# Optimization experiments

Measured on AMD Instinct MI355X. Metric: run time of the kernel, lower is better.

Reference implementation:

```python
import jax, jax.numpy as jnp
import numpy as np

B, T, IN_DIM, OUT_DIM, H = 2, 256, 512, 256, 8
TEMP = 1.0
BN_EPS = 1e-5


def _boundary_mask(bnd):
    # bnd: (B, T) float in {0,1}. Vectorized version of the nested-loop
    # construction: mask[j,k] = prod_{m=min(j,k)..max(j,k)} (1 - bnd[m]), diag=1.
    q = 1.0 - bnd  # (B, T)
    ar = jnp.arange(T)

    def per_batch(qb):
        def row(j):
            # cumprod of q starting at position j (entries before j treated as 1)
            return jnp.cumprod(jnp.where(ar >= j, qb, 1.0))
        M = jax.vmap(row)(ar)                 # (T, T); valid for k >= j
        upper = ar[None, :] >= ar[:, None]
        full = jnp.where(upper, M, M.T)       # symmetrize
        eye = ar[None, :] == ar[:, None]
        return jnp.where(eye, 1.0, full)      # diagonal forced to 1

    return jax.vmap(per_batch)(q)             # (B, T, T)


def setup_inputs() -> dict:
    key = jax.random.key(0)
    ks = jax.random.split(key, 8)
    s_in = 1.0 / np.sqrt(IN_DIM)
    s_hin = 1.0 / np.sqrt(H * IN_DIM)
    return {
        "x": jax.random.normal(ks[0], (B, T, IN_DIM), dtype=jnp.float32),
        "boundary": jax.random.randint(ks[1], (B, T), 0, 2, dtype=jnp.int32),
        "att_proj_w": jax.random.normal(ks[2], (OUT_DIM, IN_DIM), dtype=jnp.float32) * s_in,
        "att_proj_b": jnp.zeros((OUT_DIM,), dtype=jnp.float32),
        "att_weight": jax.random.normal(ks[3], (OUT_DIM, H), dtype=jnp.float32) * (1.0 / np.sqrt(OUT_DIM)),
        "proj_att_w": jax.random.normal(ks[4], (OUT_DIM, H * IN_DIM), dtype=jnp.float32) * s_hin,
        "proj_att_b": jnp.zeros((OUT_DIM,), dtype=jnp.float32),
        "proj_noatt_w": jax.random.normal(ks[5], (OUT_DIM, IN_DIM), dtype=jnp.float32) * s_in,
        "proj_noatt_b": jnp.zeros((OUT_DIM,), dtype=jnp.float32),
        "bn_gamma": jnp.ones((OUT_DIM,), dtype=jnp.float32),
        "bn_beta": jnp.zeros((OUT_DIM,), dtype=jnp.float32),
    }


def reference(x, boundary, att_proj_w, att_proj_b, att_weight,
              proj_att_w, proj_att_b, proj_noatt_w, proj_noatt_b,
              bn_gamma, bn_beta):
    bnd = boundary.astype(x.dtype)

    # pairwise node products: (B, T, T, IN_DIM)
    pm = x[:, :, None, :] * x[:, None, :, :]
    # attention logits: tanh(Linear) @ att_weight -> (B, T, T, H)
    a = jnp.tanh(jnp.einsum('bjkd,od->bjko', pm, att_proj_w) + att_proj_b)
    att = jnp.einsum('bjko,oh->bjkh', a, att_weight) / TEMP

    # boundary message-control mask, then softmax over the key-node axis (dim=-2)
    mask = _boundary_mask(bnd)                 # (B, T, T)
    att = att * mask[..., None]
    att = jax.nn.softmax(att, axis=-2)

    # aggregate per head; torch flattens (IN_DIM, H) -> IN_DIM*H with d-major order
    x1 = jnp.einsum('bjkh,bkd->bjdh', att, x).reshape(x.shape[0], x.shape[1], -1)
    x1 = x1 @ proj_att_w.T + proj_att_b
    x2 = x @ proj_noatt_w.T + proj_noatt_b
    y = x1 + x2                                # (B, T, OUT_DIM)

    # BatchNorm1d in training mode over flattened (B*T, OUT_DIM), biased variance
    flat = y.reshape(-1, y.shape[-1])
    mu = flat.mean(axis=0)
    var = flat.var(axis=0)
    yn = (flat - mu) * jax.lax.rsqrt(var + BN_EPS) * bn_gamma + bn_beta
    return jax.nn.selu(yn.reshape(y.shape))
```

## Files before the change

### kernel.cpp

```cpp
#include <hip/hip_runtime.h>
#include <hip/hip_bf16.h>

#define B_ 2
#define T_ 256
#define D_ 512
#define O_ 256
#define H_ 8

typedef __attribute__((ext_vector_type(4))) float f32x4;
typedef __attribute__((ext_vector_type(8))) short bf16x8;
typedef unsigned short u16;
typedef unsigned int u32;

__device__ __forceinline__ u16 f2b(float f) {
    u32 u = __builtin_bit_cast(u32, f);
    u32 r = (u + 0x7FFFu + ((u >> 16) & 1u)) >> 16;
    return (u16)r;
}
__device__ __forceinline__ u32 cvtpk(float lo, float hi) {
    u32 r;
    asm("v_cvt_pk_bf16_f32 %0, %1, %2" : "=v"(r) : "v"(lo), "v"(hi));
    return r;
}
__device__ __forceinline__ float fast_tanh(float x) {
    float ax = fabsf(x);
    float e = __expf(-2.f * ax);
    float r = (1.f - e) / (1.f + e);
    return x < 0.f ? -r : r;
}
__device__ __forceinline__ uint4 ld8f2b(const float* __restrict__ p) {
    f32x4 a = *reinterpret_cast<const f32x4*>(p);
    f32x4 b = *reinterpret_cast<const f32x4*>(p + 4);
    uint4 pk;
    pk.x = cvtpk(a[0], a[1]);
    pk.y = cvtpk(a[2], a[3]);
    pk.z = cvtpk(b[0], b[1]);
    pk.w = cvtpk(b[2], b[3]);
    return pk;
}
__device__ __forceinline__ void gload16(const void* g, void* l) {
    __builtin_amdgcn_global_load_lds(
        (const __attribute__((address_space(1))) unsigned int*)g,
        (__attribute__((address_space(3))) unsigned int*)l, 16, 0, 0);
}

__global__ void k0_prep(const float* __restrict__ x, const float* __restrict__ W2,
                        u16* __restrict__ Xbf, u16* __restrict__ W2t) {
    const int tid = threadIdx.x;
    if (blockIdx.x < 64) {
        int base = (blockIdx.x * 256 + tid) * 16;
        uint4 o0 = ld8f2b(x + base);
        uint4 o1 = ld8f2b(x + base + 8);
        *reinterpret_cast<uint4*>(Xbf + base) = o0;
        *reinterpret_cast<uint4*>(Xbf + base + 8) = o1;
        return;
    }
    const int bx2 = blockIdx.x - 64;
    const int o0 = (bx2 >> 3) * 16;
    const int dc = bx2 & 7;
    __shared__ u16 TL[8192];
    #pragma unroll
    for (int c = 0; c < 8; ++c) {
        int i = tid * 32 + c * 4;
        int r = i >> 9, rem = i & 511;
        f32x4 v = *reinterpret_cast<const f32x4*>(
            W2 + (size_t)(o0 + r) * 4096 + dc * 512 + rem);
        int dd = rem >> 3, h0 = rem & 7;
        TL[(h0 + 0) * 1024 + r * 64 + dd] = f2b(v[0]);
        TL[(h0 + 1) * 1024 + r * 64 + dd] = f2b(v[1]);
        TL[(h0 + 2) * 1024 + r * 64 + dd] = f2b(v[2]);
        TL[(h0 + 3) * 1024 + r * 64 + dd] = f2b(v[3]);
    }
    __syncthreads();
    #pragma unroll
    for (int c = 0; c < 4; ++c) {
        int jj = tid * 32 + c * 8;
        int h = jj >> 10, r = (jj >> 6) & 15, dd = jj & 63;
        *reinterpret_cast<uint4*>(W2t + (size_t)(h * 256 + o0 + r) * 512 + dc * 64 + dd) =
            *reinterpret_cast<const uint4*>(&TL[jj]);
    }
}

__launch_bounds__(256, 3)
__global__ void k1a_att(const u16* __restrict__ Xbf, const float* __restrict__ xf,
                        const float* __restrict__ Wap, const float* __restrict__ bap,
                        const float* __restrict__ aw, float* __restrict__ attpart)
{
    const int oc = blockIdx.x & 3;
    const int j = (blockIdx.x >> 2) & 255;
    const int b = blockIdx.x >> 10;
    const int jt = j >> 6;
    const int tid = threadIdx.x;
    const int w = tid >> 6;
    const int l = tid & 63;
    const int l15 = l & 15;
    const int lgp = l >> 4;
    const bool act = (w >= jt);

    __shared__ __align__(16) u16 XL[256 * 64];
    __shared__ __align__(16) u16 WL[64 * 72];
    __shared__ __align__(16) u16 awT[16 * 72];
    __shared__ float xj[512];

    const u16* xb = Xbf + b * (T_ * D_);
    const float* xjp = xf + (b * T_ + j) * D_;
    for (int i = tid; i < D_; i += 256) xj[i] = xjp[i];
    for (int i = tid; i < 16 * 72; i += 256) awT[i] = 0;
    __syncthreads();
    for (int i = tid; i < 64 * 8; i += 256) {
        int ol = i >> 3, h = i & 7;
        awT[h * 72 + ol] = f2b(aw[(oc * 64 + ol) * 8 + h]);
    }

    const int srow_off = (l >> 3);
    const int scol = ((l & 7) ^ ((l >> 3) & 7)) * 8;
    const int i0 = jt * 2;

    f32x4 acc[4][4] = {};
    for (int d0 = 0; d0 < D_; d0 += 64) {
        __syncthreads();
        #pragma unroll
        for (int i = 0; i < 8; ++i) {
            if (i >= i0) {
                int row = i * 32 + w * 8 + srow_off;
                gload16(xb + row * 512 + d0 + scol, &XL[i * 2048 + w * 512]);
            }
        }
        #pragma unroll
        for (int c = 0; c < 2; ++c) {
            int cc = tid + c * 256;
            int r = cc >> 3, s = cc & 7;
            const float* wp = Wap + (oc * 64 + r) * 512 + d0 + s * 8;
            f32x4 va = *reinterpret_cast<const f32x4*>(wp);
            f32x4 vb = *reinterpret_cast<const f32x4*>(wp + 4);
            f32x4 xa = *reinterpret_cast<const f32x4*>(&xj[d0 + s * 8]);
            f32x4 xc = *reinterpret_cast<const f32x4*>(&xj[d0 + s * 8 + 4]);
            uint4 pk;
            pk.x = cvtpk(va[0] * xa[0], va[1] * xa[1]);
            pk.y = cvtpk(va[2] * xa[2], va[3] * xa[3]);
            pk.z = cvtpk(vb[0] * xc[0], vb[1] * xc[1]);
            pk.w = cvtpk(vb[2] * xc[2], vb[3] * xc[3]);
            *reinterpret_cast<uint4*>(&WL[r * 72 + s * 8]) = pk;
        }
        __syncthreads();
        if (act) {
            #pragma unroll
            for (int ds = 0; ds < 2; ++ds) {
                bf16x8 wfr[4];
                #pragma unroll
                for (int ot = 0; ot < 4; ++ot)
                    wfr[ot] = *reinterpret_cast<const bf16x8*>(&WL[(ot * 16 + l15) * 72 + ds * 32 + lgp * 8]);
                #pragma unroll
                for (int kt = 0; kt < 4; ++kt) {
                    int row = w * 64 + kt * 16 + l15;
                    int c16 = ((ds * 4 + lgp) ^ (l15 & 7)) * 8;
                    bf16x8 xfr = *reinterpret_cast<const bf16x8*>(&XL[row * 64 + c16]);
                    #pragma unroll
                    for (int ot = 0; ot < 4; ++ot)
                        acc[ot][kt] = __builtin_amdgcn_mfma_f32_16x16x32_bf16(wfr[ot], xfr, acc[ot][kt], 0, 0, 0);
                }
            }
        }
    }
    u16* a_lds = XL;
    if (act) {
        #pragma unroll
        for (int ot = 0; ot < 4; ++ot) {
            f32x4 bv = *reinterpret_cast<const f32x4*>(bap + oc * 64 + ot * 16 + lgp * 4);
            #pragma unroll
            for (int kt = 0; kt < 4; ++kt) {
                int k = w * 64 + kt * 16 + l15;
                float t0 = fast_tanh(acc[ot][kt][0] + bv[0]);
                float t1 = fast_tanh(acc[ot][kt][1] + bv[1]);
                float t2 = fast_tanh(acc[ot][kt][2] + bv[2]);
                float t3 = fast_tanh(acc[ot][kt][3] + bv[3]);
                uint2 pk;
                pk.x = cvtpk(t0, t1);
                pk.y = cvtpk(t2, t3);
                int c16 = (ot * 2 + (lgp >> 1)) ^ (l15 & 7);
                *reinterpret_cast<uint2*>(&a_lds[k * 64 + c16 * 8 + (lgp & 1) * 4]) = pk;
            }
        }
    }
    f32x4 attacc[4] = {};
    if (act) {
        #pragma unroll
        for (int ds = 0; ds < 2; ++ds) {
            bf16x8 bw = *reinterpret_cast<const bf16x8*>(&awT[l15 * 72 + ds * 32 + lgp * 8]);
            #pragma unroll
            for (int kt = 0; kt < 4; ++kt) {
                int row = w * 64 + kt * 16 + l15;
                int c16 = ((ds * 4 + lgp) ^ (l15 & 7)) * 8;
                bf16x8 af = *reinterpret_cast<const bf16x8*>(&a_lds[row * 64 + c16]);
                attacc[kt] = __builtin_amdgcn_mfma_f32_16x16x32_bf16(af, bw, attacc[kt], 0, 0, 0);
            }
        }
        float* dst = attpart + ((size_t)blockIdx.x) * 256 * 8;
        #pragma unroll
        for (int kt = 0; kt < 4; ++kt) {
            if (l15 < 8) {
                #pragma unroll
                for (int i = 0; i < 4; ++i) {
                    int k = w * 64 + kt * 16 + lgp * 4 + i;
                    dst[k * 8 + l15] = attacc[kt][i];
                }
            }
        }
        if (w > jt && l15 < 8) {
            #pragma unroll
            for (int kt = 0; kt < 4; ++kt) {
                #pragma unroll
                for (int i = 0; i < 4; ++i) {
                    int k = w * 64 + kt * 16 + lgp * 4 + i;
                    attpart[(((size_t)(b * 256 + k)) * 4 + oc) * 2048 + j * 8 + l15] = attacc[kt][i];
                }
            }
        }
    }
}

__global__ void k1b_sm(const float* __restrict__ attpart, const int* __restrict__ bnd,
                       u16* __restrict__ P2)
{
    const int b = blockIdx.x >> 8;
    const int j = blockIdx.x & 255;
    const int tid = threadIdx.x;

    __shared__ float attL[256 * 9];
    __shared__ float maskv[256];
    __shared__ int scanv[256];

    scanv[tid] = bnd[b * T_ + tid];
    __syncthreads();
    for (int off = 1; off < 256; off <<= 1) {
        int v = (tid >= off) ? scanv[tid - off] : 0;
        __syncthreads();
        scanv[tid] += v;
        __syncthreads();
    }
    {
        int k = tid;
        float m;
        if (k == j) m = 1.f;
        else if (k > j) m = ((scanv[k] - (j ? scanv[j - 1] : 0)) == 0) ? 1.f : 0.f;
        else m = ((scanv[j] - (k ? scanv[k - 1] : 0)) == 0) ? 1.f : 0.f;
        maskv[k] = m;
    }
    {
        const float* base = attpart + ((size_t)(b * 256 + j) * 4) * 256 * 8 + tid * 8;
        f32x4 s0 = *reinterpret_cast<const f32x4*>(base);
        f32x4 s1 = *reinterpret_cast<const f32x4*>(base + 4);
        #pragma unroll
        for (int oc = 1; oc < 4; ++oc) {
            s0 += *reinterpret_cast<const f32x4*>(base + (size_t)oc * 2048);
            s1 += *reinterpret_cast<const f32x4*>(base + (size_t)oc * 2048 + 4);
        }
        #pragma unroll
        for (int e = 0; e < 4; ++e) attL[tid * 9 + e] = s0[e];
        #pragma unroll
        for (int e = 0; e < 4; ++e) attL[tid * 9 + 4 + e] = s1[e];
    }
    __syncthreads();

    {
        int h = tid >> 5, c = tid & 31;
        float lgv[8];
        float mx = -3.4e38f;
        #pragma unroll
        for (int kk = 0; kk < 8; ++kk) {
            int k = c + kk * 32;
            float v = attL[k * 9 + h] * maskv[k];
            lgv[kk] = v;
            mx = fmaxf(mx, v);
        }
        #pragma unroll
        for (int off = 1; off < 32; off <<= 1)
            mx = fmaxf(mx, __shfl_xor(mx, off, 32));
        float sum = 0.f;
        #pragma unroll
        for (int kk = 0; kk < 8; ++kk) {
            lgv[kk] = __expf(lgv[kk] - mx);
            sum += lgv[kk];
        }
        #pragma unroll
        for (int off = 1; off < 32; off <<= 1)
            sum += __shfl_xor(sum, off, 32);
        float inv = 1.f / sum;
        u16* dst = P2 + ((size_t)(b * 256 + j)) * 2048 + h * 256;
        #pragma unroll
        for (int kk = 0; kk < 8; ++kk)
            dst[c + kk * 32] = f2b(lgv[kk] * inv);
    }
}

__launch_bounds__(256, 4)
__global__ void k2m_mm(const u16* __restrict__ Xbf, const u16* __restrict__ W2t,
                       u16* __restrict__ M)
{
    const int kh = blockIdx.x & 1;
    const int on = (blockIdx.x >> 1) & 15;
    const int h = (blockIdx.x >> 5) & 7;
    const int b = blockIdx.x >> 8;
    const int tid = threadIdx.x;
    const int w = tid >> 6, l = tid & 63, l15 = l & 15, lgp = l >> 4;

    __shared__ __align__(16) u16 XL[128 * 64];
    __shared__ __align__(16) u16 WL[16 * 72];

    const u16* xb = Xbf + b * (T_ * D_) + kh * 128 * D_;
    const int srow_off = (l >> 3);
    const int scol = ((l & 7) ^ ((l >> 3) & 7)) * 8;

    f32x4 acc[2] = {};
    for (int d0 = 0; d0 < D_; d0 += 64) {
        __syncthreads();
        #pragma unroll
        for (int i = 0; i < 4; ++i) {
            int row = i * 32 + w * 8 + srow_off;
            gload16(xb + row * 512 + d0 + scol, &XL[i * 2048 + w * 512]);
        }
        if (tid < 128) {
            int r = tid >> 3, s = tid & 7;
            *reinterpret_cast<uint4*>(&WL[r * 72 + s * 8]) =
                *reinterpret_cast<const uint4*>(
                    W2t + (size_t)(h * 256 + on * 16 + r) * 512 + d0 + s * 8);
        }
        __syncthreads();
        #pragma unroll
        for (int ds = 0; ds < 2; ++ds) {
            bf16x8 bfr = *reinterpret_cast<const bf16x8*>(&WL[l15 * 72 + ds * 32 + lgp * 8]);
            #pragma unroll
            for (int kt = 0; kt < 2; ++kt) {
                int row = w * 32 + kt * 16 + l15;
                int c16 = ((ds * 4 + lgp) ^ (l15 & 7)) * 8;
                bf16x8 afr = *reinterpret_cast<const bf16x8*>(&XL[row * 64 + c16]);
                acc[kt] = __builtin_amdgcn_mfma_f32_16x16x32_bf16(afr, bfr, acc[kt], 0, 0, 0);
            }
        }
    }
    u16* dst = M + ((size_t)(b * 8 + h) * 256 + on * 16 + l15) * 256 + kh * 128;
    #pragma unroll
    for (int kt = 0; kt < 2; ++kt) {
        uint2 pk;
        pk.x = cvtpk(acc[kt][0], acc[kt][1]);
        pk.y = cvtpk(acc[kt][2], acc[kt][3]);
        *reinterpret_cast<uint2*>(dst + w * 32 + kt * 16 + lgp * 4) = pk;
    }
}

__launch_bounds__(256, 4)
__global__ void k3_mm(const u16* __restrict__ P2, const u16* __restrict__ M,
                      const u16* __restrict__ Xbf, const float* __restrict__ W3,
                      float* __restrict__ part)
{
    const int gid = blockIdx.x;
    const int tid = threadIdx.x;
    const int w = tid >> 6, l = tid & 63, l15 = l & 15, lgp = l >> 4;

    __shared__ __align__(16) u16 AL[64 * 72];
    __shared__ __align__(16) u16 BL[64 * 72];

    f32x4 acc[4] = {};
    int jc, oc, slot;
    if (gid < 128) {
        int kc = gid & 3;
        oc = (gid >> 2) & 3;
        jc = gid >> 4;
        slot = kc;
        const int j0 = jc * 64, o0 = oc * 64;
        const int bb = jc >> 2;
        for (int t = 0; t < 8; ++t) {
            const int hh = kc * 2 + (t >> 2);
            const int k0 = (t & 3) * 64;
            __syncthreads();
            #pragma unroll
            for (int c = 0; c < 2; ++c) {
                int cc = tid + c * 256;
                int r = cc >> 3, s = cc & 7;
                *reinterpret_cast<uint4*>(&AL[r * 72 + s * 8]) =
                    *reinterpret_cast<const uint4*>(
                        P2 + (size_t)(j0 + r) * 2048 + hh * 256 + k0 + s * 8);
                *reinterpret_cast<uint4*>(&BL[r * 72 + s * 8]) =
                    *reinterpret_cast<const uint4*>(
                        M + ((size_t)(bb * 8 + hh) * 256 + o0 + r) * 256 + k0 + s * 8);
            }
            __syncthreads();
            #pragma unroll
            for (int ds = 0; ds < 2; ++ds) {
                bf16x8 afr = *reinterpret_cast<const bf16x8*>(&AL[(w * 16 + l15) * 72 + ds * 32 + lgp * 8]);
                #pragma unroll
                for (int ot = 0; ot < 4; ++ot) {
                    bf16x8 bfr = *reinterpret_cast<const bf16x8*>(&BL[(ot * 16 + l15) * 72 + ds * 32 + lgp * 8]);
                    acc[ot] = __builtin_amdgcn_mfma_f32_16x16x32_bf16(afr, bfr, acc[ot], 0, 0, 0);
                }
            }
        }
    } else {
        int g2 = gid - 128;
        oc = g2 & 3;
        jc = g2 >> 2;
        slot = 4;
        const int j0 = jc * 64, o0 = oc * 64;
        for (int t0 = 0; t0 < 512; t0 += 64) {
            __syncthreads();
            #pragma unroll
            for (int c = 0; c < 2; ++c) {
                int cc = tid + c * 256;
                int r = cc >> 3, s = cc & 7;
                *reinterpret_cast<uint4*>(&AL[r * 72 + s * 8]) =
                    *reinterpret_cast<const uint4*>(Xbf + (size_t)(j0 + r) * 512 + t0 + s * 8);
                *reinterpret_cast<uint4*>(&BL[r * 72 + s * 8]) =
                    ld8f2b(W3 + (size_t)(o0 + r) * 512 + t0 + s * 8);
            }
            __syncthreads();
            #pragma unroll
            for (int ds = 0; ds < 2; ++ds) {
                bf16x8 afr = *reinterpret_cast<const bf16x8*>(&AL[(w * 16 + l15) * 72 + ds * 32 + lgp * 8]);
                #pragma unroll
                for (int ot = 0; ot < 4; ++ot) {
                    bf16x8 bfr = *reinterpret_cast<const bf16x8*>(&BL[(ot * 16 + l15) * 72 + ds * 32 + lgp * 8]);
                    acc[ot] = __builtin_amdgcn_mfma_f32_16x16x32_bf16(afr, bfr, acc[ot], 0, 0, 0);
                }
            }
        }
    }
    const int j0 = jc * 64, o0 = oc * 64;
    float* dst = part + (size_t)slot * 512 * 256;
    #pragma unroll
    for (int ot = 0; ot < 4; ++ot)
        #pragma unroll
        for (int i = 0; i < 4; ++i) {
            int rr = j0 + w * 16 + lgp * 4 + i;
            int o = o0 + ot * 16 + l15;
            dst[rr * 256 + o] = acc[ot][i];
        }
}

__global__ void k4a_comb(const float* __restrict__ part,
                         const float* __restrict__ pb2, const float* __restrict__ pb3,
                         float* __restrict__ ypre,
                         float* __restrict__ psum, float* __restrict__ psq)
{
    int g = blockIdx.x, o = threadIdx.x;
    float bsum = pb2[o] + pb3[o];
    float s = 0.f, q = 0.f;
    for (int r = g * 8; r < g * 8 + 8; ++r) {
        size_t idx = (size_t)r * 256 + o;
        float v = part[idx] + part[131072 + idx] + part[2 * 131072 + idx]
                + part[3 * 131072 + idx] + part[4 * 131072 + idx] + bsum;
        ypre[idx] = v;
        s += v; q += v * v;
    }
    psum[g * 256 + o] = s;
    psq[g * 256 + o] = q;
}

__global__ void k4b_norm(const float* __restrict__ ypre,
                         const float* __restrict__ psum, const float* __restrict__ psq,
                         const float* __restrict__ gamma, const float* __restrict__ beta,
                         float* __restrict__ out) {
    int r = blockIdx.x, o = threadIdx.x;
    float s = 0.f, q = 0.f;
    #pragma unroll 8
    for (int g = 0; g < 64; ++g) {
        s += psum[g * 256 + o];
        q += psq[g * 256 + o];
    }
    float mu = s * (1.f / 512.f);
    float var = q * (1.f / 512.f) - mu * mu;
    float inv = rsqrtf(var + 1e-5f);
    float v = (ypre[r * 256 + o] - mu) * inv * gamma[o] + beta[o];
    const float SC = 1.0507009873554805f, AL = 1.6732632423543772f;
    float ov = v > 0.f ? SC * v : SC * AL * (__expf(v) - 1.f);
    out[r * 256 + o] = ov;
}

extern "C" void kernel_launch(void* const* d_in, const int* in_sizes, int n_in,
                              void* d_out, int out_size, void* d_ws, size_t ws_size,
                              hipStream_t stream) {
    const float* x    = (const float*)d_in[0];
    const int* bnd    = (const int*)d_in[1];
    const float* Wap  = (const float*)d_in[2];
    const float* bap  = (const float*)d_in[3];
    const float* aw   = (const float*)d_in[4];
    const float* W2   = (const float*)d_in[5];
    const float* pb2  = (const float*)d_in[6];
    const float* W3   = (const float*)d_in[7];
    const float* pb3  = (const float*)d_in[8];
    const float* gamma = (const float*)d_in[9];
    const float* beta  = (const float*)d_in[10];
    float* out = (float*)d_out;
    (void)in_sizes; (void)n_in; (void)out_size; (void)ws_size;

    char* ws = (char*)d_ws;
    u16* Xbf   = (u16*)ws;  ws += (size_t)B_ * T_ * D_ * 2;
    u16* W2t   = (u16*)ws;  ws += (size_t)H_ * O_ * D_ * 2;
    u16* P2    = (u16*)ws;  ws += (size_t)B_ * T_ * H_ * T_ * 2;
    u16* Mbuf  = (u16*)ws;  ws += (size_t)B_ * H_ * O_ * T_ * 2;
    float* part = (float*)ws; ws += (size_t)5 * 512 * 256 * 4;
    float* ypre = (float*)ws; ws += (size_t)B_ * T_ * O_ * 4;
    float* psum = (float*)ws; ws += (size_t)64 * O_ * 4;
    float* psq  = (float*)ws; ws += (size_t)64 * O_ * 4;
    float* attpart = (float*)ws; ws += (size_t)2048 * 256 * 8 * 4;

    k0_prep<<<192, 256, 0, stream>>>(x, W2, Xbf, W2t);
    k1a_att<<<2048, 256, 0, stream>>>(Xbf, x, Wap, bap, aw, attpart);
    k1b_sm<<<512, 256, 0, stream>>>(attpart, bnd, P2);
    k2m_mm<<<512, 256, 0, stream>>>(Xbf, W2t, Mbuf);
    k3_mm<<<160, 256, 0, stream>>>(P2, Mbuf, Xbf, W3, part);
    k4a_comb<<<64, 256, 0, stream>>>(part, pb2, pb3, ypre, psum, psq);
    k4b_norm<<<512, 256, 0, stream>>>(ypre, psum, psq, gamma, beta, out);
}
```

Baseline: 88.83 us.

## Trim k1a LDS footprint for higher occupancy and hoist boundary scan into prep

The attention-logit kernel drops its LDS copies of x_j and the transposed head weights, keeping the head weights as register fragments and reading x_j directly from global memory. WL is shrunk to an XOR-swizzled unpadded layout, and the launch-bounds occupancy hint is raised from 3 to 4 blocks per CU. The boundary prefix scan moves out of every softmax block into two extra prep blocks that write the scan to global memory, so 512 blocks no longer each repeat an 8-step barrier loop. The tradeoff is higher register pressure under the tighter occupancy bound, which could cause spills, plus repeated global loads of x_j.

```diff
diff --git a/kernel.cpp b/kernel.cpp
--- a/kernel.cpp
+++ b/kernel.cpp
@@ -45,7 +45,9 @@
 }
 
 __global__ void k0_prep(const float* __restrict__ x, const float* __restrict__ W2,
-                        u16* __restrict__ Xbf, u16* __restrict__ W2t) {
+                        const int* __restrict__ bnd,
+                        u16* __restrict__ Xbf, u16* __restrict__ W2t,
+                        int* __restrict__ scan_g) {
     const int tid = threadIdx.x;
     if (blockIdx.x < 64) {
         int base = (blockIdx.x * 256 + tid) * 16;
@@ -53,6 +55,20 @@
         uint4 o1 = ld8f2b(x + base + 8);
         *reinterpret_cast<uint4*>(Xbf + base) = o0;
         *reinterpret_cast<uint4*>(Xbf + base + 8) = o1;
+        return;
+    }
+    if (blockIdx.x >= 192) {
+        const int b = blockIdx.x - 192;
+        __shared__ int sc[256];
+        sc[tid] = bnd[b * 256 + tid];
+        __syncthreads();
+        for (int off = 1; off < 256; off <<= 1) {
+            int v = (tid >= off) ? sc[tid - off] : 0;
+            __syncthreads();
+            sc[tid] += v;
+            __syncthreads();
+        }
+        scan_g[b * 256 + tid] = sc[tid];
         return;
     }
     const int bx2 = blockIdx.x - 64;
@@ -81,7 +97,7 @@
     }
 }
 
-__launch_bounds__(256, 3)
+__launch_bounds__(256, 4)
 __global__ void k1a_att(const u16* __restrict__ Xbf, const float* __restrict__ xf,
                         const float* __restrict__ Wap, const float* __restrict__ bap,
                         const float* __restrict__ aw, float* __restrict__ attpart)
@@ -98,23 +114,26 @@
     const bool act = (w >= jt);
 
     __shared__ __align__(16) u16 XL[256 * 64];
-    __shared__ __align__(16) u16 WL[64 * 72];
-    __shared__ __align__(16) u16 awT[16 * 72];
-    __shared__ float xj[512];
+    __shared__ __align__(16) u16 WL[64 * 64];
 
     const u16* xb = Xbf + b * (T_ * D_);
     const float* xjp = xf + (b * T_ + j) * D_;
-    for (int i = tid; i < D_; i += 256) xj[i] = xjp[i];
-    for (int i = tid; i < 16 * 72; i += 256) awT[i] = 0;
-    __syncthreads();
-    for (int i = tid; i < 64 * 8; i += 256) {
-        int ol = i >> 3, h = i & 7;
-        awT[h * 72 + ol] = f2b(aw[(oc * 64 + ol) * 8 + h]);
+
+    bf16x8 bwreg[2];
+    #pragma unroll
+    for (int ds = 0; ds < 2; ++ds) {
+        u16 awtmp[8];
+        #pragma unroll
+        for (int e = 0; e < 8; ++e)
+            awtmp[e] = (l15 < 8) ? f2b(aw[(oc * 64 + ds * 32 + lgp * 8 + e) * 8 + l15]) : (u16)0;
+        bwreg[ds] = *reinterpret_cast<const bf16x8*>(awtmp);
     }
 
     const int srow_off = (l >> 3);
     const int scol = ((l & 7) ^ ((l >> 3) & 7)) * 8;
     const int i0 = jt * 2;
+    const int wr0 = tid >> 3, wsc = (tid & 7) * 8;
+    const int wswz0 = ((tid & 7) ^ (wr0 & 7)) * 8;
 
     f32x4 acc[4][4] = {};
     for (int d0 = 0; d0 < D_; d0 += 64) {
@@ -126,21 +145,26 @@
                 gload16(xb + row * 512 + d0 + scol, &XL[i * 2048 + w * 512]);
             }
         }
-        #pragma unroll
-        for (int c = 0; c < 2; ++c) {
-            int cc = tid + c * 256;
-            int r = cc >> 3, s = cc & 7;
-            const float* wp = Wap + (oc * 64 + r) * 512 + d0 + s * 8;
-            f32x4 va = *reinterpret_cast<const f32x4*>(wp);
-            f32x4 vb = *reinterpret_cast<const f32x4*>(wp + 4);
-            f32x4 xa = *reinterpret_cast<const f32x4*>(&xj[d0 + s * 8]);
-            f32x4 xc = *reinterpret_cast<const f32x4*>(&xj[d0 + s * 8 + 4]);
+        {
+            f32x4 xa = *reinterpret_cast<const f32x4*>(xjp + d0 + wsc);
+            f32x4 xc = *reinterpret_cast<const f32x4*>(xjp + d0 + wsc + 4);
+            const float* wp0 = Wap + (size_t)(oc * 64 + wr0) * 512 + d0 + wsc;
+            f32x4 va = *reinterpret_cast<const f32x4*>(wp0);
+            f32x4 vb = *reinterpret_cast<const f32x4*>(wp0 + 4);
             uint4 pk;
             pk.x = cvtpk(va[0] * xa[0], va[1] * xa[1]);
             pk.y = cvtpk(va[2] * xa[2], va[3] * xa[3]);
             pk.z = cvtpk(vb[0] * xc[0], vb[1] * xc[1]);
             pk.w = cvtpk(vb[2] * xc[2], vb[3] * xc[3]);
-            *reinterpret_cast<uint4*>(&WL[r * 72 + s * 8]) = pk;
+            *reinterpret_cast<uint4*>(&WL[wr0 * 64 + wswz0]) = pk;
+            const float* wp1 = wp0 + 32 * 512;
+            va = *reinterpret_cast<const f32x4*>(wp1);
+            vb = *reinterpret_cast<const f32x4*>(wp1 + 4);
+            pk.x = cvtpk(va[0] * xa[0], va[1] * xa[1]);
+            pk.y = cvtpk(va[2] * xa[2], va[3] * xa[3]);
+            pk.z = cvtpk(vb[0] * xc[0], vb[1] * xc[1]);
+            pk.w = cvtpk(vb[2] * xc[2], vb[3] * xc[3]);
+            *reinterpret_cast<uint4*>(&WL[(wr0 + 32) * 64 + wswz0]) = pk;
         }
         __syncthreads();
         if (act) {
@@ -148,8 +172,10 @@
             for (int ds = 0; ds < 2; ++ds) {
                 bf16x8 wfr[4];
                 #pragma unroll
-                for (int ot = 0; ot < 4; ++ot)
-                    wfr[ot] = *reinterpret_cast<const bf16x8*>(&WL[(ot * 16 + l15) * 72 + ds * 32 + lgp * 8]);
+                for (int ot = 0; ot < 4; ++ot) {
+                    int wc = ((ds * 4 + lgp) ^ (l15 & 7)) * 8;
+                    wfr[ot] = *reinterpret_cast<const bf16x8*>(&WL[(ot * 16 + l15) * 64 + wc]);
+                }
                 #pragma unroll
                 for (int kt = 0; kt < 4; ++kt) {
                     int row = w * 64 + kt * 16 + l15;
@@ -186,13 +212,12 @@
     if (act) {
         #pragma unroll
         for (int ds = 0; ds < 2; ++ds) {
-            bf16x8 bw = *reinterpret_cast<const bf16x8*>(&awT[l15 * 72 + ds * 32 + lgp * 8]);
             #pragma unroll
             for (int kt = 0; kt < 4; ++kt) {
                 int row = w * 64 + kt * 16 + l15;
                 int c16 = ((ds * 4 + lgp) ^ (l15 & 7)) * 8;
                 bf16x8 af = *reinterpret_cast<const bf16x8*>(&a_lds[row * 64 + c16]);
-                attacc[kt] = __builtin_amdgcn_mfma_f32_16x16x32_bf16(af, bw, attacc[kt], 0, 0, 0);
+                attacc[kt] = __builtin_amdgcn_mfma_f32_16x16x32_bf16(af, bwreg[ds], attacc[kt], 0, 0, 0);
             }
         }
         float* dst = attpart + ((size_t)blockIdx.x) * 256 * 8;
@@ -219,7 +244,7 @@
     }
 }
 
-__global__ void k1b_sm(const float* __restrict__ attpart, const int* __restrict__ bnd,
+__global__ void k1b_sm(const float* __restrict__ attpart, const int* __restrict__ scan_g,
                        u16* __restrict__ P2)
 {
     const int b = blockIdx.x >> 8;
@@ -228,22 +253,14 @@
 
     __shared__ float attL[256 * 9];
     __shared__ float maskv[256];
-    __shared__ int scanv[256];
-
-    scanv[tid] = bnd[b * T_ + tid];
-    __syncthreads();
-    for (int off = 1; off < 256; off <<= 1) {
-        int v = (tid >= off) ? scanv[tid - off] : 0;
-        __syncthreads();
-        scanv[tid] += v;
-        __syncthreads();
-    }
+
     {
         int k = tid;
+        const int* sg = scan_g + b * 256;
         float m;
         if (k == j) m = 1.f;
-        else if (k > j) m = ((scanv[k] - (j ? scanv[j - 1] : 0)) == 0) ? 1.f : 0.f;
-        else m = ((scanv[j] - (k ? scanv[k - 1] : 0)) == 0) ? 1.f : 0.f;
+        else if (k > j) m = ((sg[k] - (j ? sg[j - 1] : 0)) == 0) ? 1.f : 0.f;
+        else m = ((sg[j] - (k ? sg[k - 1] : 0)) == 0) ? 1.f : 0.f;
         maskv[k] = m;
     }
     {
@@ -501,11 +518,12 @@
     float* ypre = (float*)ws; ws += (size_t)B_ * T_ * O_ * 4;
     float* psum = (float*)ws; ws += (size_t)64 * O_ * 4;
     float* psq  = (float*)ws; ws += (size_t)64 * O_ * 4;
+    int* scan_g = (int*)ws;  ws += (size_t)B_ * T_ * 4;
     float* attpart = (float*)ws; ws += (size_t)2048 * 256 * 8 * 4;
 
-    k0_prep<<<192, 256, 0, stream>>>(x, W2, Xbf, W2t);
+    k0_prep<<<194, 256, 0, stream>>>(x, W2, bnd, Xbf, W2t, scan_g);
     k1a_att<<<2048, 256, 0, stream>>>(Xbf, x, Wap, bap, aw, attpart);
-    k1b_sm<<<512, 256, 0, stream>>>(attpart, bnd, P2);
+    k1b_sm<<<512, 256, 0, stream>>>(attpart, scan_g, P2);
     k2m_mm<<<512, 256, 0, stream>>>(Xbf, W2t, Mbuf);
     k3_mm<<<160, 256, 0, stream>>>(P2, Mbuf, Xbf, W3, part);
     k4a_comb<<<64, 256, 0, stream>>>(part, pb2, pb3, ypre, psum, psq);
```

New measurement: 88.74 us (median of 2 runs). About the same (-0.1%).
